# Kernel tuning notes

Measured on AMD Instinct MI355X. Metric: run time of the kernel, lower is better.

The kernel has to match this reference:

```python
import jax, jax.numpy as jnp
import numpy as np

SEQ = 4096
D = 1024      # input_dim
DK = 1024     # query_dim
DV = 1024     # encoding_dim
STD = 0.02


def setup_inputs() -> dict:
    key = jax.random.key(0)
    kz, kq, kk, kv = jax.random.split(key, 4)
    z = jax.random.normal(kz, (SEQ, D), dtype=jnp.float32)
    # weights stored as [in, out], matching q = z @ Wq
    Wq = STD * jax.random.normal(kq, (D, DK), dtype=jnp.float32)
    Wk = STD * jax.random.normal(kk, (D, DK), dtype=jnp.float32)
    Wv = STD * jax.random.normal(kv, (D, DV), dtype=jnp.float32)
    return {"z": z, "Wq": Wq, "Wk": Wk, "Wv": Wv}


def reference(z, Wq, Wk, Wv):
    q = z @ Wq                      # [S, dk]
    k = z @ Wk                      # [S, dk]
    v = z @ Wv                      # [S, dv]
    # NOTE: original applies the 1/sqrt(dk) scale AFTER softmax (to the probabilities)
    attn = jax.nn.softmax(q @ k.T, axis=-1) * (DK ** -0.5)  # [S, S]
    return attn @ v                 # [S, dv]
```

## Files before the change

kernel.cpp:

```cpp
#include <hip/hip_runtime.h>

typedef unsigned short u16;
typedef unsigned int u32;
typedef __attribute__((ext_vector_type(8))) short bf16x8;
typedef __attribute__((ext_vector_type(8))) _Float16 f16x8;
typedef __attribute__((ext_vector_type(4))) float f32x4;

__device__ inline u16 f2bf(float f){
  union { float f; unsigned u; } v; v.f = f;
  unsigned r = v.u + 0x7FFFu + ((v.u >> 16) & 1u);
  return (u16)(r >> 16);
}
__device__ inline float bf2f(u16 u){
  union { unsigned u; float f; } v; v.u = ((unsigned)u) << 16;
  return v.f;
}
__device__ inline u16 f2h(float f){
  union { _Float16 h; u16 u; } v; v.h = (_Float16)f; return v.u;
}

__device__ inline void gload16(const u16* g, u16* l){
  __builtin_amdgcn_global_load_lds(
      (const __attribute__((address_space(1))) u32*)(const void*)g,
      (__attribute__((address_space(3))) u32*)(void*)l, 16, 0, 0);
}

#define WAITV(n) asm volatile("s_waitcnt vmcnt(" #n ")" ::: "memory")
#define FENCE()  asm volatile("" ::: "memory")

__global__ __launch_bounds__(256) void split_f32(const float* __restrict__ x,
                                                 u16* __restrict__ hi,
                                                 u16* __restrict__ lo, int n4){
  int i = blockIdx.x * 256 + threadIdx.x;
  if (i >= n4) return;
  float4 v = ((const float4*)x)[i];
  float a0 = v.x, a1 = v.y, a2 = v.z, a3 = v.w;
  u16 h0 = f2bf(a0), h1 = f2bf(a1), h2 = f2bf(a2), h3 = f2bf(a3);
  ushort4 h; h.x = h0; h.y = h1; h.z = h2; h.w = h3;
  ushort4 l; l.x = f2bf(a0 - bf2f(h0)); l.y = f2bf(a1 - bf2f(h1));
  l.z = f2bf(a2 - bf2f(h2)); l.w = f2bf(a3 - bf2f(h3));
  ((ushort4*)hi)[i] = h;
  ((ushort4*)lo)[i] = l;
}

__global__ __launch_bounds__(256) void split_z(const float* __restrict__ x,
                                               u16* __restrict__ hi,
                                               u16* __restrict__ h16, int n4){
  int i = blockIdx.x * 256 + threadIdx.x;
  if (i >= n4) return;
  float4 v = ((const float4*)x)[i];
  ushort4 h; h.x = f2bf(v.x); h.y = f2bf(v.y); h.z = f2bf(v.z); h.w = f2bf(v.w);
  ushort4 g; g.x = f2h(v.x); g.y = f2h(v.y); g.z = f2h(v.z); g.w = f2h(v.w);
  ((ushort4*)hi)[i] = h;
  ((ushort4*)h16)[i] = g;
}

__global__ __launch_bounds__(256) void transpose_wv(
    const float* __restrict__ W, u16* __restrict__ H){
  __shared__ float t[64][65];
  int d0 = blockIdx.y * 64, n0 = blockIdx.x * 64;
  int tid = threadIdx.x;
  int r = tid >> 4, c4 = (tid & 15) * 4;
  for (int rr = r; rr < 64; rr += 16){
    float4 v = *(const float4*)&W[(size_t)(d0 + rr) * 1024 + n0 + c4];
    t[rr][c4 + 0] = v.x; t[rr][c4 + 1] = v.y; t[rr][c4 + 2] = v.z; t[rr][c4 + 3] = v.w;
  }
  __syncthreads();
  int n = tid >> 4, d4 = (tid & 15) * 4;
  for (int nn = n; nn < 64; nn += 16){
    ushort4 h;
    h.x = f2bf(t[d4 + 0][nn]); h.y = f2bf(t[d4 + 1][nn]);
    h.z = f2bf(t[d4 + 2][nn]); h.w = f2bf(t[d4 + 3][nn]);
    *(ushort4*)&H[(size_t)(n0 + nn) * 1024 + d0 + d4] = h;
  }
}

template<int IN, int EPI>
__global__ __launch_bounds__(256) void gemm_bt(
    const u16* __restrict__ Ah, const u16* __restrict__ Al, int lda,
    const u16* __restrict__ Bh, const u16* __restrict__ Bl, int ldb,
    void* __restrict__ C0, int ldc, int K, size_t zslab){
  constexpr int NPL = (IN == 0) ? 4 : 2;
  constexpr int DEPTH = (IN == 0) ? 1 : 2;
  constexpr int NBUF = DEPTH + 1;
  __shared__ __align__(16) u16 sm[NBUF * NPL * 4096];

  const int kz = blockIdx.z * K;
  Ah += kz; Bh += kz;
  if constexpr (IN == 0){ Al += kz; Bl += kz; }

  const int tid = threadIdx.x;
  const int lane = tid & 63, wave = tid >> 6;
  const int wr = wave >> 1, wc = wave & 1;
  const int lr = lane & 15, kg = lane >> 4;

  const int nwg = gridDim.x * gridDim.y;
  const int id = blockIdx.y * gridDim.x + blockIdx.x;
  const int chunk = nwg >> 3;
  const int swz = (id & 7) * chunk + (id >> 3);
  const int bx = swz % gridDim.x, by = swz / gridDim.x;
  const int m0 = by * 128, n0 = bx * 128;

  const int l_r = lane >> 2, l_c = lane & 3;
  const int st_chunk = l_c ^ ((l_r + (l_r >> 2)) & 3);
  const int rd_swz = (lr + (lr >> 2)) & 3;

  f32x4 acc[4][4];
  #pragma unroll
  for (int m = 0; m < 4; m++)
    #pragma unroll
    for (int n = 0; n < 4; n++)
      acc[m][n] = (f32x4){0.f, 0.f, 0.f, 0.f};

  auto STAGE = [&](int buf, int k0){
    #pragma unroll
    for (int c = 0; c < NPL * 2; ++c){
      int pc = c * 4 + wave;
      int p = pc >> 3, ch = pc & 7;
      const u16* g; int ld, rb;
      if (IN == 0){
        g = (p == 0) ? Ah : (p == 1) ? Al : (p == 2) ? Bh : Bl;
        ld = (p < 2) ? lda : ldb;  rb = (p < 2) ? m0 : n0;
      } else {
        g = (p == 0) ? Ah : Bh;
        ld = (p == 0) ? lda : ldb; rb = (p == 0) ? m0 : n0;
      }
      int r = ch * 16 + l_r;
      const u16* src = g + (size_t)(rb + r) * ld + k0 + st_chunk * 8;
      u16* dst = &sm[((size_t)buf * NPL + p) * 4096 + ch * 512];
      gload16(src, dst);
    }
  };

  const int KT = K >> 5;
  STAGE(0, 0);
  if constexpr (DEPTH == 2){ if (KT > 1) STAGE(1, 32); }

  int bufc = 0, pfb = DEPTH % NBUF;
  for (int kt = 0; kt < KT; ++kt){
    const int pf = kt + DEPTH;
    if (pf < KT){
      STAGE(pfb, pf * 32);
      WAITV(8);
    } else if (kt + 1 < KT){
      if constexpr (IN == 0) WAITV(8); else WAITV(4);
    } else {
      WAITV(0);
    }
    __builtin_amdgcn_s_barrier();
    FENCE();

    const u16* pA  = &sm[((size_t)bufc * NPL + 0) * 4096];
    const u16* pAl = &sm[((size_t)bufc * NPL + 1) * 4096];
    const u16* pB  = &sm[((size_t)bufc * NPL + (IN == 0 ? 2 : 1)) * 4096];
    const u16* pBl = &sm[((size_t)bufc * NPL + 3) * 4096];

    const int slot = (kg ^ rd_swz) * 8;
    bf16x8 afh[4], bfh[4], afl[4], bfl[4];
    f16x8 ah16[4], bh16[4];
    #pragma unroll
    for (int m = 0; m < 4; m++){
      int r = wr * 64 + m * 16 + lr;
      if (IN == 2) ah16[m] = *(const f16x8*)&pA[r * 32 + slot];
      else {
        afh[m] = *(const bf16x8*)&pA[r * 32 + slot];
        if (IN == 0) afl[m] = *(const bf16x8*)&pAl[r * 32 + slot];
      }
    }
    #pragma unroll
    for (int n = 0; n < 4; n++){
      int r = wc * 64 + n * 16 + lr;
      if (IN == 2) bh16[n] = *(const f16x8*)&pB[r * 32 + slot];
      else {
        bfh[n] = *(const bf16x8*)&pB[r * 32 + slot];
        if (IN == 0) bfl[n] = *(const bf16x8*)&pBl[r * 32 + slot];
      }
    }
    #pragma unroll
    for (int m = 0; m < 4; m++)
      #pragma unroll
      for (int n = 0; n < 4; n++){
        if (IN == 2){
          acc[m][n] = __builtin_amdgcn_mfma_f32_16x16x32_f16(ah16[m], bh16[n], acc[m][n], 0, 0, 0);
        } else {
          acc[m][n] = __builtin_amdgcn_mfma_f32_16x16x32_bf16(afh[m], bfh[n], acc[m][n], 0, 0, 0);
          if (IN == 0){
            acc[m][n] = __builtin_amdgcn_mfma_f32_16x16x32_bf16(afl[m], bfh[n], acc[m][n], 0, 0, 0);
            acc[m][n] = __builtin_amdgcn_mfma_f32_16x16x32_bf16(afh[m], bfl[n], acc[m][n], 0, 0, 0);
          }
        }
      }
    FENCE();
    __builtin_amdgcn_s_barrier();
    bufc = (bufc + 1 == NBUF) ? 0 : bufc + 1;
    pfb  = (pfb  + 1 == NBUF) ? 0 : pfb  + 1;
  }

  const int row0 = m0 + wr * 64, col0 = n0 + wc * 64 + lr;
  #pragma unroll
  for (int m = 0; m < 4; m++)
    #pragma unroll
    for (int n = 0; n < 4; n++)
      #pragma unroll
      for (int r = 0; r < 4; r++){
        int row = row0 + m * 16 + kg * 4 + r;
        int col = col0 + n * 16;
        float x = acc[m][n][r];
        if (EPI == 0){
          float* C = (float*)C0 + (size_t)blockIdx.z * zslab;
          C[(size_t)row * ldc + col] = x;
        } else {
          ((u16*)C0)[(size_t)row * ldc + col] = f2h(x);
        }
      }
}

__global__ __launch_bounds__(512, 1) void gemm256(
    const u16* __restrict__ A, int lda,
    const u16* __restrict__ B, int ldb,
    float* __restrict__ C0z, int l0, float* __restrict__ C1z, int l1,
    float* __restrict__ C2z, int l2, float* __restrict__ C3z, int l3,
    int K){
  __shared__ __align__(16) u16 sm[2 * 32768];

  const int tid = threadIdx.x;
  const int lane = tid & 63, wave = tid >> 6;
  const int wr = wave >> 2, wc = wave & 3;
  const int lr = lane & 15, kg = lane >> 4;
  const int g7 = lr & 7;

  const int nwg = gridDim.x * gridDim.y;
  const int id = blockIdx.y * gridDim.x + blockIdx.x;
  const int chunk = nwg >> 3;
  const int swz = (id & 7) * chunk + (id >> 3);
  const int bx = swz % gridDim.x, by = swz / gridDim.x;
  const int m0 = by * 256, n0 = bx * 256;

  A += (size_t)blockIdx.z * (size_t)K;
  B += (size_t)blockIdx.z * (size_t)K;
  float* Cp; int ldc;
  if (blockIdx.z == 0){ Cp = C0z; ldc = l0; }
  else if (blockIdx.z == 1){ Cp = C1z; ldc = l1; }
  else if (blockIdx.z == 2){ Cp = C2z; ldc = l2; }
  else { Cp = C3z; ldc = l3; }

  auto STAGE = [&](int buf, int k0){
    #pragma unroll
    for (int rd = 0; rd < 8; ++rd){
      int p = rd >> 2;
      int r0 = (rd & 3) * 64 + wave * 8;
      const u16* g = p ? B : A;
      int ld = p ? ldb : lda;
      int rb = p ? n0 : m0;
      int grow = rb + r0 + (lane >> 3);
      int gch = (lane & 7) ^ (lane >> 3);
      const u16* src = g + (size_t)grow * ld + k0 + gch * 8;
      u16* dst = &sm[(size_t)buf * 32768 + p * 16384 + r0 * 64];
      gload16(src, dst);
    }
  };

  f32x4 acc[8][4];
  #pragma unroll
  for (int m = 0; m < 8; m++)
    #pragma unroll
    for (int n = 0; n < 4; n++)
      acc[m][n] = (f32x4){0.f, 0.f, 0.f, 0.f};

  const int KT = K >> 6;
  STAGE(0, 0);

  int bufc = 0;
  for (int kt = 0; kt < KT; ++kt){
    WAITV(0);
    __builtin_amdgcn_s_barrier();
    FENCE();
    if (kt + 1 < KT) STAGE(bufc ^ 1, (kt + 1) * 64);

    const u16* pA = &sm[(size_t)bufc * 32768];
    const u16* pB = pA + 16384;
    #pragma unroll
    for (int ks = 0; ks < 2; ++ks){
      f16x8 b[4], a[8];
      #pragma unroll
      for (int n = 0; n < 4; n++){
        int R = wc * 64 + n * 16 + lr;
        b[n] = *(const f16x8*)&pB[R * 64 + (((ks * 4 + kg) ^ g7) * 8)];
      }
      #pragma unroll
      for (int m = 0; m < 8; m++){
        int R = wr * 128 + m * 16 + lr;
        a[m] = *(const f16x8*)&pA[R * 64 + (((ks * 4 + kg) ^ g7) * 8)];
      }
      __builtin_amdgcn_s_setprio(1);
      #pragma unroll
      for (int m = 0; m < 8; m++)
        #pragma unroll
        for (int n = 0; n < 4; n++)
          acc[m][n] = __builtin_amdgcn_mfma_f32_16x16x32_f16(a[m], b[n], acc[m][n], 0, 0, 0);
      __builtin_amdgcn_s_setprio(0);
    }
    FENCE();
    bufc ^= 1;
  }

  const int row0 = m0 + wr * 128, col0 = n0 + wc * 64 + lr;
  #pragma unroll
  for (int m = 0; m < 8; m++)
    #pragma unroll
    for (int n = 0; n < 4; n++)
      #pragma unroll
      for (int r = 0; r < 4; r++){
        int row = row0 + m * 16 + kg * 4 + r;
        int col = col0 + n * 16;
        Cp[(size_t)row * ldc + col] = acc[m][n][r];
      }
}

__global__ __launch_bounds__(256) void reduce_t(u16* __restrict__ dst,
                                                const float* __restrict__ s0,
                                                const float* __restrict__ s1,
                                                const float* __restrict__ s2,
                                                const float* __restrict__ s3){
  int idx = blockIdx.x * 256 + threadIdx.x;
  float4 a = ((const float4*)s0)[idx];
  float4 b = ((const float4*)s1)[idx];
  float4 c = ((const float4*)s2)[idx];
  float4 d = ((const float4*)s3)[idx];
  ushort4 o;
  o.x = f2h((a.x + b.x) + (c.x + d.x));
  o.y = f2h((a.y + b.y) + (c.y + d.y));
  o.z = f2h((a.z + b.z) + (c.z + d.z));
  o.w = f2h((a.w + b.w) + (c.w + d.w));
  ((ushort4*)dst)[idx] = o;
}

__global__ __launch_bounds__(256) void reduce_pv(float* __restrict__ out,
                                                 const float* __restrict__ Sf,
                                                 const float* __restrict__ s3){
  int idx = blockIdx.x * 256 + threadIdx.x;
  int r = idx >> 8, c4 = (idx & 255) * 4;
  float4 a = ((const float4*)out)[idx];
  float4 b = ((const float4*)s3)[idx];
  float4 h1 = *(const float4*)&Sf[(size_t)r * 4096 + 2048 + c4];
  float4 h2 = *(const float4*)&Sf[(size_t)r * 4096 + 3072 + c4];
  float4 o;
  o.x = (a.x + b.x) + (h1.x + h2.x);
  o.y = (a.y + b.y) + (h1.y + h2.y);
  o.z = (a.z + b.z) + (h1.z + h2.z);
  o.w = (a.w + b.w) + (h1.w + h2.w);
  ((float4*)out)[idx] = o;
}

__global__ __launch_bounds__(256) void softmax_rows(float* __restrict__ S){
  int rrow = blockIdx.x;
  float* srow = S + (size_t)rrow * 4096;
  __shared__ float e[4096];
  __shared__ float red[4];
  int tid = threadIdx.x;

  float m = -1e30f;
  for (int i = tid * 4; i < 4096; i += 1024){
    float4 v = *(const float4*)(srow + i);
    m = fmaxf(m, fmaxf(fmaxf(v.x, v.y), fmaxf(v.z, v.w)));
  }
  for (int o = 32; o > 0; o >>= 1) m = fmaxf(m, __shfl_xor(m, o));
  if ((tid & 63) == 0) red[tid >> 6] = m;
  __syncthreads();
  m = fmaxf(fmaxf(red[0], red[1]), fmaxf(red[2], red[3]));

  float s = 0.f;
  for (int i = tid * 4; i < 4096; i += 1024){
    float4 v = *(const float4*)(srow + i);
    float4 ev;
    ev.x = __expf(v.x - m); ev.y = __expf(v.y - m);
    ev.z = __expf(v.z - m); ev.w = __expf(v.w - m);
    s += (ev.x + ev.y) + (ev.z + ev.w);
    *(float4*)&e[i] = ev;
  }
  for (int o = 32; o > 0; o >>= 1) s += __shfl_xor(s, o);
  __syncthreads();
  if ((tid & 63) == 0) red[tid >> 6] = s;
  __syncthreads();
  s = (red[0] + red[1]) + (red[2] + red[3]);

  float scale = 0.03125f / s;
  u16* prow = (u16*)((char*)S + (size_t)rrow * 16384);
  for (int i = tid * 4; i < 4096; i += 1024){
    float4 v = *(const float4*)&e[i];
    ushort4 o; o.x = f2h(v.x * scale); o.y = f2h(v.y * scale);
    o.z = f2h(v.z * scale); o.w = f2h(v.w * scale);
    *(ushort4*)(prow + i) = o;
  }
}

extern "C" void kernel_launch(void* const* d_in, const int* in_sizes, int n_in,
                              void* d_out, int out_size, void* d_ws, size_t ws_size,
                              hipStream_t stream){
  const float* z  = (const float*)d_in[0];
  const float* Wq = (const float*)d_in[1];
  const float* Wk = (const float*)d_in[2];
  const float* Wv = (const float*)d_in[3];
  char* ws = (char*)d_ws;
  const size_t MB = 1ull << 20;

  u16* t16   = (u16*)(ws + 0 * MB);
  u16* z16   = (u16*)(ws + 8 * MB);
  u16* vt16  = (u16*)(ws + 16 * MB);
  float* S   = (float*)(ws + 24 * MB);
  u16* m16   = (u16*)(ws + 88 * MB);
  float* slab3 = (float*)(ws + 0 * MB);
  float* ts0 = (float*)(ws + 24 * MB);
  float* ts1 = (float*)(ws + 40 * MB);
  float* ts2 = (float*)(ws + 56 * MB);
  float* ts3 = (float*)(ws + 72 * MB);
  u16* z_hi  = (u16*)(ws + 24 * MB);
  u16* wqh   = (u16*)(ws + 32 * MB);
  u16* wql   = (u16*)(ws + 34 * MB);
  u16* wkh   = (u16*)(ws + 36 * MB);
  u16* wkl   = (u16*)(ws + 38 * MB);
  float* msl = (float*)(ws + 40 * MB);
  u16* wvt_h = (u16*)(ws + 56 * MB);

  split_z<<<4096, 256, 0, stream>>>(z, z_hi, z16, 4096 * 1024 / 4);
  split_f32<<<1024, 256, 0, stream>>>(Wq, wqh, wql, 1024 * 1024 / 4);
  split_f32<<<1024, 256, 0, stream>>>(Wk, wkh, wkl, 1024 * 1024 / 4);
  transpose_wv<<<dim3(16, 16), 256, 0, stream>>>(Wv, wvt_h);

  gemm_bt<0, 0><<<dim3(8, 8, 4), 256, 0, stream>>>(wkh, wkl, 1024,
      wqh, wql, 1024, msl, 1024, 256, (size_t)1024 * 1024);
  reduce_t<<<1024, 256, 0, stream>>>(m16, msl, msl + 1048576,
      msl + 2097152, msl + 3145728);

  gemm_bt<1, 1><<<dim3(32, 8), 256, 0, stream>>>(wvt_h, nullptr, 1024,
      z_hi, nullptr, 1024, vt16, 4096, 1024, 0);

  gemm_bt<2, 0><<<dim3(8, 32, 4), 256, 0, stream>>>(z16, nullptr, 1024,
      m16, nullptr, 1024, ts0, 1024, 256, (size_t)4096 * 1024);
  reduce_t<<<4096, 256, 0, stream>>>(t16, ts0, ts1, ts2, ts3);

  gemm256<<<dim3(16, 16, 1), 512, 0, stream>>>(t16, 1024, z16, 1024,
      S, 4096, S, 4096, S, 4096, S, 4096, 1024);

  softmax_rows<<<4096, 256, 0, stream>>>(S);

  gemm256<<<dim3(4, 16, 4), 512, 0, stream>>>((u16*)S, 8192, vt16, 4096,
      (float*)d_out, 1024, S + 2048, 4096, S + 3072, 4096, slab3, 1024, 1024);

  reduce_pv<<<4096, 256, 0, stream>>>((float*)d_out, S, slab3);
}
```

Before: 192.0 us.

## Use fp16 for V projection and drop split-K with reduction for T

Converts z only to fp16 and transposes Wv to fp16, so the V projection runs through the fp16 GEMM path and the separate bf16 copy of z is no longer produced. The T = z·M GEMM now writes fp16 output directly from a single-pass launch instead of four split-K slabs followed by a reduce kernel. This removes one kernel launch and the fp32 slab traffic, at the cost of less parallelism for the T GEMM and fp16 range and precision risk in V.

```diff
diff --git a/kernel.cpp b/kernel.cpp
--- a/kernel.cpp
+++ b/kernel.cpp
@@ -43,19 +43,16 @@
   ((ushort4*)lo)[i] = l;
 }
 
-__global__ __launch_bounds__(256) void split_z(const float* __restrict__ x,
-                                               u16* __restrict__ hi,
-                                               u16* __restrict__ h16, int n4){
+__global__ __launch_bounds__(256) void conv_h16(const float* __restrict__ x,
+                                                u16* __restrict__ h16, int n4){
   int i = blockIdx.x * 256 + threadIdx.x;
   if (i >= n4) return;
   float4 v = ((const float4*)x)[i];
-  ushort4 h; h.x = f2bf(v.x); h.y = f2bf(v.y); h.z = f2bf(v.z); h.w = f2bf(v.w);
   ushort4 g; g.x = f2h(v.x); g.y = f2h(v.y); g.z = f2h(v.z); g.w = f2h(v.w);
-  ((ushort4*)hi)[i] = h;
   ((ushort4*)h16)[i] = g;
 }
 
-__global__ __launch_bounds__(256) void transpose_wv(
+__global__ __launch_bounds__(256) void transpose_wv16(
     const float* __restrict__ W, u16* __restrict__ H){
   __shared__ float t[64][65];
   int d0 = blockIdx.y * 64, n0 = blockIdx.x * 64;
@@ -69,8 +66,8 @@
   int n = tid >> 4, d4 = (tid & 15) * 4;
   for (int nn = n; nn < 64; nn += 16){
     ushort4 h;
-    h.x = f2bf(t[d4 + 0][nn]); h.y = f2bf(t[d4 + 1][nn]);
-    h.z = f2bf(t[d4 + 2][nn]); h.w = f2bf(t[d4 + 3][nn]);
+    h.x = f2h(t[d4 + 0][nn]); h.y = f2h(t[d4 + 1][nn]);
+    h.z = f2h(t[d4 + 2][nn]); h.w = f2h(t[d4 + 3][nn]);
     *(ushort4*)&H[(size_t)(n0 + nn) * 1024 + d0 + d4] = h;
   }
 }
@@ -410,34 +407,28 @@
   float* S   = (float*)(ws + 24 * MB);
   u16* m16   = (u16*)(ws + 88 * MB);
   float* slab3 = (float*)(ws + 0 * MB);
-  float* ts0 = (float*)(ws + 24 * MB);
-  float* ts1 = (float*)(ws + 40 * MB);
-  float* ts2 = (float*)(ws + 56 * MB);
-  float* ts3 = (float*)(ws + 72 * MB);
-  u16* z_hi  = (u16*)(ws + 24 * MB);
-  u16* wqh   = (u16*)(ws + 32 * MB);
-  u16* wql   = (u16*)(ws + 34 * MB);
-  u16* wkh   = (u16*)(ws + 36 * MB);
-  u16* wkl   = (u16*)(ws + 38 * MB);
+  u16* wqh   = (u16*)(ws + 24 * MB);
+  u16* wql   = (u16*)(ws + 26 * MB);
+  u16* wkh   = (u16*)(ws + 28 * MB);
+  u16* wkl   = (u16*)(ws + 30 * MB);
+  u16* wvt16 = (u16*)(ws + 32 * MB);
   float* msl = (float*)(ws + 40 * MB);
-  u16* wvt_h = (u16*)(ws + 56 * MB);
-
-  split_z<<<4096, 256, 0, stream>>>(z, z_hi, z16, 4096 * 1024 / 4);
+
+  conv_h16<<<4096, 256, 0, stream>>>(z, z16, 4096 * 1024 / 4);
   split_f32<<<1024, 256, 0, stream>>>(Wq, wqh, wql, 1024 * 1024 / 4);
   split_f32<<<1024, 256, 0, stream>>>(Wk, wkh, wkl, 1024 * 1024 / 4);
-  transpose_wv<<<dim3(16, 16), 256, 0, stream>>>(Wv, wvt_h);
+  transpose_wv16<<<dim3(16, 16), 256, 0, stream>>>(Wv, wvt16);
 
   gemm_bt<0, 0><<<dim3(8, 8, 4), 256, 0, stream>>>(wkh, wkl, 1024,
       wqh, wql, 1024, msl, 1024, 256, (size_t)1024 * 1024);
   reduce_t<<<1024, 256, 0, stream>>>(m16, msl, msl + 1048576,
       msl + 2097152, msl + 3145728);
 
-  gemm_bt<1, 1><<<dim3(32, 8), 256, 0, stream>>>(wvt_h, nullptr, 1024,
-      z_hi, nullptr, 1024, vt16, 4096, 1024, 0);
-
-  gemm_bt<2, 0><<<dim3(8, 32, 4), 256, 0, stream>>>(z16, nullptr, 1024,
-      m16, nullptr, 1024, ts0, 1024, 256, (size_t)4096 * 1024);
-  reduce_t<<<4096, 256, 0, stream>>>(t16, ts0, ts1, ts2, ts3);
+  gemm_bt<2, 1><<<dim3(32, 8), 256, 0, stream>>>(wvt16, nullptr, 1024,
+      z16, nullptr, 1024, vt16, 4096, 1024, 0);
+
+  gemm_bt<2, 1><<<dim3(8, 32), 256, 0, stream>>>(z16, nullptr, 1024,
+      m16, nullptr, 1024, t16, 1024, 1024, 0);
 
   gemm256<<<dim3(16, 16, 1), 512, 0, stream>>>(t16, 1024, z16, 1024,
       S, 4096, S, 4096, S, 4096, S, 4096, 1024);
```

Measured after the change: 176.2 us. -8.3%, faster.
